# Optimization experiments

Hardware: AMD Instinct MI355X
Metric: run time of the kernel (lower is better)

Reference implementation:

```python
import jax, jax.numpy as jnp
import numpy as np
import math

D_MODEL = 1024
N_HEADS = 16
HEAD_DIM = D_MODEL // N_HEADS
B, S = 4, 4096


def setup_inputs() -> dict:
    key = jax.random.key(0)
    ks = jax.random.split(key, 8)
    # xavier-uniform-ish scale for square DxD matrices
    lim = math.sqrt(6.0 / (D_MODEL + D_MODEL))
    def W(k):
        return jax.random.uniform(k, (D_MODEL, D_MODEL), jnp.float32, -lim, lim)
    return {
        "x": jax.random.normal(ks[0], (B, S, D_MODEL), jnp.float32),
        "fractal_dim": jnp.float32(1.7),
        "Wq": W(ks[1]), "bq": jnp.zeros((D_MODEL,), jnp.float32),
        "Wk": W(ks[2]), "bk": jnp.zeros((D_MODEL,), jnp.float32),
        "Wv": W(ks[3]), "bv": jnp.zeros((D_MODEL,), jnp.float32),
        "Wo": W(ks[4]), "bo": jnp.zeros((D_MODEL,), jnp.float32),
        "alpha": jnp.float32(1.5),
        "frac_scale": jnp.float32(0.5),
    }


def reference(x, fractal_dim, Wq, bq, Wk, bk, Wv, bv, Wo, bo, alpha, frac_scale):
    b, s, d = x.shape
    h, hd = N_HEADS, HEAD_DIM
    residual = x

    adaptive_alpha = alpha + frac_scale * (fractal_dim - 1.5)

    q = (x @ Wq + bq).reshape(b, s, h, hd)
    k = (x @ Wk + bk).reshape(b, s, h, hd)
    v = (x @ Wv + bv).reshape(b, s, h, hd)

    # spectral filter over frequency axis (seq dim)
    freqs = jnp.fft.fftfreq(s).astype(x.dtype)  # [S]
    phase = adaptive_alpha * jnp.arctan(jnp.log(jnp.abs(freqs) + 1e-10))
    filt = jnp.exp(1j * phase)[None, :, None, None]  # [1,S,1,1] complex

    def spectral(t):
        tf = jnp.fft.fft(t, axis=1, norm="ortho") * filt
        return jnp.fft.ifft(tf, axis=1, norm="ortho").real

    q_t, k_t, v_t = spectral(q), spectral(k), spectral(v)

    # per-(token) dot product across head_dim -> logits over heads
    logits = jnp.einsum("bshd,bshd->bsh", q_t, k_t) / math.sqrt(hd)
    w = jax.nn.softmax(logits, axis=-1)  # softmax over heads
    attended = w[..., None] * v_t  # [B,S,H,Hd]

    # final inverse FFT of the (real) attended signal along seq dim
    attended_time = jnp.fft.ifft(attended.astype(jnp.complex64), axis=1, norm="ortho").real

    out = attended_time.reshape(b, s, d) @ Wo + bo
    return out + residual
```

## Files before the change

### kernel.cpp

```cpp
#include <hip/hip_runtime.h>

#define S      4096
#define DM     1024
#define NB     4
#define NH     16
#define HDIM   64
#define MTOT   (NB * S)
#define DS     ((long)DM * S)
#define MH     2304
#define KH     2112
#define KH2    2112
#define MEO    2048

typedef __attribute__((ext_vector_type(8))) short short8;
typedef __attribute__((ext_vector_type(4))) float f32x4;
typedef __attribute__((ext_vector_type(8))) unsigned short u16x8;
typedef __attribute__((ext_vector_type(4))) unsigned short u16x4;

__device__ __forceinline__ unsigned short f2bf(float f) {
  union { float f; unsigned u; } v; v.f = f;
  unsigned r = v.u + 0x7fffu + ((v.u >> 16) & 1u);
  return (unsigned short)(r >> 16);
}
__device__ __forceinline__ float bf2f(short h) {
  union { unsigned u; float f; } v; v.u = ((unsigned)(unsigned short)h) << 16;
  return v.f;
}

#define GLOAD(gp, lp) __builtin_amdgcn_global_load_lds( \
    (const __attribute__((address_space(1))) void*)(gp), \
    (__attribute__((address_space(3))) void*)(lp), 16, 0, 0)

#define SBAR() do { asm volatile("" ::: "memory"); __builtin_amdgcn_s_barrier(); \
                    asm volatile("" ::: "memory"); } while (0)
#define WAITL0() asm volatile("s_waitcnt lgkmcnt(0)" ::: "memory")

#define SWZ(o) ((o) ^ ((((o) >> 7) & 3) << 4))


__global__ void k_tables(const float* __restrict__ fd, const float* __restrict__ alpha,
                         const float* __restrict__ fsc,
                         float* __restrict__ cos_tab, float* __restrict__ c_arr) {
  int k = blockIdx.x * 256 + threadIdx.x;
  if (k >= S) return;
  float aa = alpha[0] + fsc[0] * (fd[0] - 1.5f);
  const float twopi = 6.28318530717958647692f;
  cos_tab[k] = cosf(twopi * ((float)k / (float)S));
  int kk = (k <= S / 2) ? k : (S - k);
  float af = (float)kk / (float)S;
  c_arr[k] = cosf(aa * atanf(logf(af + 1e-10f)));
}

__global__ void k_g(const float* __restrict__ cos_tab, const float* __restrict__ c_arr,
                    float* __restrict__ g) {
  __shared__ float sct[S];
  __shared__ float sc[S];
  __shared__ float red[16][17];
  for (int i = threadIdx.x; i < S; i += 256) { sct[i] = cos_tab[i]; sc[i] = c_arr[i]; }
  __syncthreads();
  int jl = threadIdx.x >> 4, r = threadIdx.x & 15;
  int j = blockIdx.x * 16 + jl;
  float acc = 0.f;
#pragma unroll 4
  for (int i = 0; i < 256; ++i) {
    int k = r + 16 * i;
    acc += sc[k] * sct[(j * k) & (S - 1)];
  }
  red[jl][r] = acc;
  __syncthreads();
  if (r == 0) {
    float s = 0.f;
#pragma unroll
    for (int i = 0; i < 16; ++i) s += red[jl][i];
    g[j] = s * (1.f / (float)S);
  }
}

__global__ void k_buildEO(const float* __restrict__ g, short* __restrict__ Ge) {
  long i8 = ((long)blockIdx.x * 256 + threadIdx.x) * 8;
  if (i8 >= (long)MEO * KH2) return;
  int n = (int)(i8 / KH2);
  int m = (int)(i8 % KH2);
  u16x8 ev, ov;
#pragma unroll
  for (int j = 0; j < 8; ++j) {
    int mm = m + j;
    float e, o;
    if (mm == 0)            { e = g[n]; o = 0.f; }
    else if (mm == 2048)    { e = g[(n + 2048) & (S - 1)]; o = 0.f; }
    else if (mm > 2048)     { e = 0.f; o = 0.f; }
    else {
      float a = g[(n - mm) & (S - 1)], b = g[(n + mm) & (S - 1)];
      e = 0.5f * (a + b); o = 0.5f * (a - b);
    }
    ev[j] = f2bf(e); ov[j] = f2bf(o);
  }
  *(u16x8*)(Ge + i8) = ev;
  *(u16x8*)(Ge + (long)MEO * KH2 + i8) = ov;
}

__global__ void k_foldT(const float* __restrict__ x, short* __restrict__ uv) {
  __shared__ float tp[64][65];
  __shared__ float tm[64][65];
  int m0 = blockIdx.x * 64, d0 = blockIdx.y * 64, b = blockIdx.z;
  int t = threadIdx.x;
  int r = t >> 4, c4 = (t & 15) * 4;
#pragma unroll
  for (int rr = 0; rr < 4; ++rr) {
    int m = m0 + r + rr * 16;
    float4 vp = *(const float4*)(x + ((long)(b * S + m)) * DM + d0 + c4);
    int ms = (S - m) & (S - 1);
    float4 vm = *(const float4*)(x + ((long)(b * S + ms)) * DM + d0 + c4);
    tp[r + rr * 16][c4 + 0] = vp.x; tp[r + rr * 16][c4 + 1] = vp.y;
    tp[r + rr * 16][c4 + 2] = vp.z; tp[r + rr * 16][c4 + 3] = vp.w;
    tm[r + rr * 16][c4 + 0] = vm.x; tm[r + rr * 16][c4 + 1] = vm.y;
    tm[r + rr * 16][c4 + 2] = vm.z; tm[r + rr * 16][c4 + 3] = vm.w;
  }
  __syncthreads();
  int m_loc = t & 63, dq = t >> 6;
#pragma unroll
  for (int i = 0; i < 16; ++i) {
    int d_loc = dq * 16 + i;
    int m = m0 + m_loc;
    float P = tp[m_loc][d_loc], M = tm[m_loc][d_loc];
    float u, v;
    if (m == 0 || m == 2048) { u = P; v = 0.f; }
    else if (m > 2048)       { u = 0.f; v = 0.f; }
    else                     { u = P + M; v = P - M; }
    long base = ((long)(b * DM + d0 + d_loc)) * KH2 + m;
    uv[base] = (short)f2bf(u);
    uv[base + (long)4 * DM * KH2] = (short)f2bf(v);
  }
}

__global__ void k_row2048(const float* __restrict__ g, const short* __restrict__ uv,
                          short* __restrict__ Xs) {
  __shared__ float red[256];
  int bd = blockIdx.x;
  int b = bd >> 10, d = bd & (DM - 1);
  const short* up = uv + ((long)(b * DM + d)) * KH2;
  int t = threadIdx.x;
  float acc = 0.f;
  for (int m = t; m <= 2048; m += 256)
    acc += g[2048 - m] * bf2f(up[m]);
  red[t] = acc;
  __syncthreads();
  for (int sh = 128; sh > 0; sh >>= 1) {
    if (t < sh) red[t] += red[t + sh];
    __syncthreads();
  }
  if (t == 0) Xs[((long)b * S + 2048) * DM + d] = (short)f2bf(red[0]);
}

__global__ void k_unfold(const short* __restrict__ AB, short* __restrict__ Xs) {
  long i8 = ((long)blockIdx.x * 256 + threadIdx.x) * 8;
  if (i8 >= (long)NB * MEO * DM) return;
  int b = (int)(i8 >> 21);
  long rr = i8 & ((1L << 21) - 1);
  int n = (int)(rr >> 10);
  int d = (int)(rr & (DM - 1));
  u16x8 av = *(const u16x8*)(AB + i8);
  u16x8 bv = *(const u16x8*)(AB + ((long)4 * MEO * DM) + i8);
  u16x8 sv, dv;
#pragma unroll
  for (int j = 0; j < 8; ++j) {
    float A = bf2f((short)av[j]), B = bf2f((short)bv[j]);
    sv[j] = f2bf(A + B);
    dv[j] = f2bf(A - B);
  }
  *(u16x8*)(Xs + ((long)b * S + n) * DM + d) = sv;
  if (n > 0)
    *(u16x8*)(Xs + ((long)b * S + (S - n)) * DM + d) = dv;
}

__global__ void k_buildM2(const float* __restrict__ cos_tab, short* __restrict__ Mc2) {
  long i8 = ((long)blockIdx.x * 256 + threadIdx.x) * 8;
  if (i8 >= (long)MH * KH) return;
  int n = (int)(i8 / KH);
  int m = (int)(i8 % KH);
  u16x8 mv;
#pragma unroll
  for (int j = 0; j < 8; ++j) {
    int mm = m + j;
    float vv = (mm <= 2048) ? cos_tab[(n * mm) & (S - 1)] * 0.015625f : 0.f;
    mv[j] = f2bf(vv);
  }
  *(u16x8*)(Mc2 + i8) = mv;
}

__global__ void k_transW(const float* __restrict__ W, short* __restrict__ WT) {
  __shared__ float tile[64][65];
  int k0 = blockIdx.x * 64, n0 = blockIdx.y * 64;
  int t = threadIdx.x;
  int r = t >> 4, c4 = (t & 15) * 4;
  const float* ip = W + (long)k0 * DM + n0;
#pragma unroll
  for (int rr = 0; rr < 4; ++rr) {
    float4 v = *(const float4*)(ip + (long)(r + rr * 16) * DM + c4);
    tile[r + rr * 16][c4 + 0] = v.x;
    tile[r + rr * 16][c4 + 1] = v.y;
    tile[r + rr * 16][c4 + 2] = v.z;
    tile[r + rr * 16][c4 + 3] = v.w;
  }
  __syncthreads();
  int k_loc = t & 63, nq = t >> 6;
  short* op = WT + (long)n0 * DM + k0;
#pragma unroll
  for (int i = 0; i < 16; ++i) {
    int n_loc = nq * 16 + i;
    op[(long)n_loc * DM + k_loc] = (short)f2bf(tile[k_loc][n_loc]);
  }
}

__global__ void k_logits(const short* __restrict__ Qt, const short* __restrict__ Kt,
                         float* __restrict__ logits) {
  int s = blockIdx.x * 256 + threadIdx.x;
  int h = blockIdx.y, b = blockIdx.z;
  const short* q = Qt + ((long)b * DM + h * HDIM) * S + s;
  const short* k = Kt + ((long)b * DM + h * HDIM) * S + s;
  float acc = 0.f;
#pragma unroll 8
  for (int j = 0; j < HDIM; ++j)
    acc += bf2f(q[(long)j * S]) * bf2f(k[(long)j * S]);
  logits[((long)b * NH + h) * S + s] = acc * 0.125f;
}

__global__ void k_softw(const float* __restrict__ logits, float* __restrict__ w) {
  int idx = blockIdx.x * 256 + threadIdx.x;
  if (idx >= NB * S) return;
  int b = idx >> 12, s = idx & (S - 1);
  const float* lp = logits + (long)b * NH * S + s;
  float v[NH];
  float m = -1e30f;
#pragma unroll
  for (int h = 0; h < NH; ++h) { v[h] = lp[(long)h * S]; m = fmaxf(m, v[h]); }
  float sum = 0.f;
#pragma unroll
  for (int h = 0; h < NH; ++h) { v[h] = expf(v[h] - m); sum += v[h]; }
  float inv = 1.f / sum;
  float* wp = w + (long)b * NH * S + s;
#pragma unroll
  for (int h = 0; h < NH; ++h) wp[(long)h * S] = v[h] * inv;
}

__global__ void k_attfold(const short* __restrict__ vt, const float* __restrict__ wsm,
                          short* __restrict__ A2t) {
  int m = blockIdx.x * 256 + threadIdx.x;
  if (m >= KH) return;
  int d = blockIdx.y, b = blockIdx.z;
  const short* vp = vt + ((long)b * DM + d) * S;
  const float* wp = wsm + ((long)b * NH + (d >> 6)) * S;
  float v;
  if (m == 0) v = wp[0] * bf2f(vp[0]);
  else if (m < 2048) v = wp[m] * bf2f(vp[m]) + wp[4096 - m] * bf2f(vp[4096 - m]);
  else if (m == 2048) v = wp[2048] * bf2f(vp[2048]);
  else v = 0.f;
  A2t[((long)b * DM + d) * KH + m] = (short)f2bf(v);
}

template <int EPI, int AMIR = 0, int ASEL = 0, int WALK = 0>
__global__ __launch_bounds__(512, 2) void gemm8(
    const short* __restrict__ A, const short* __restrict__ Bt,
    short* __restrict__ Cb, short* __restrict__ Cb2, short* __restrict__ Cb3,
    float* __restrict__ Cf,
    const float* __restrict__ bias, const float* __restrict__ bias2,
    const float* __restrict__ bias3,
    const float* __restrict__ bsc, const float* __restrict__ resid,
    int M, int N, int K, long aBatch, long bBatch, long cBatch) {
  __shared__ __align__(16) short SH[65536];
  auto Ab = [&](int buf, int ks) { return SH + (buf * 2 + ks) * 8192; };
  auto Bb = [&](int buf, int ks) { return SH + 32768 + (buf * 2 + ks) * 8192; };

  const int gx = gridDim.x, gy = gridDim.y;
  const int nwg = gx * gy * gridDim.z;
  int lin = blockIdx.x + gx * (blockIdx.y + gy * blockIdx.z);
  int wg = lin;
  if ((nwg & 7) == 0) {
    const int cpx = nwg >> 3;
    wg = (lin & 7) * cpx + (lin >> 3);
  }
  const int NTN = N >> 8;
  const int NTM = M >> 8;
  int ntile, mtile, bz;
  if (WALK) {
    mtile = wg % NTM;
    const int rest = wg / NTM;
    ntile = rest % NTN;
    bz = rest / NTN;
  } else {
    ntile = wg % NTN;
    const int rest = wg / NTN;
    mtile = rest % NTM;
    bz = rest / NTM;
  }

  const short* Ag = ASEL ? (A + (long)(bz >> 2) * aBatch) : (A + (long)bz * aBatch);
  const short* Bg = Bt + (long)bz * bBatch;
  const int m0 = mtile << 8, n0 = ntile << 8;
  const int tid = threadIdx.x;
  const int lane = tid & 63;
  const int wid = tid >> 6;
  const int wm = wid >> 2, wn = wid & 3;

  f32x4 acc[8][4];
#pragma unroll
  for (int i = 0; i < 8; ++i)
#pragma unroll
    for (int j = 0; j < 4; ++j) acc[i][j] = (f32x4){0.f, 0.f, 0.f, 0.f};

  const int NT = K >> 6;
  auto stage = [&](int h) {
    const int tau = h >> 2, q = h & 3;
    const int buf = tau & 1, ks = q >> 1;
    short* ldsbase = (q & 1) ? Bb(buf, ks) : Ab(buf, ks);
    const short* gsrc = (q & 1) ? Bg : Ag;
    const int row0 = (q & 1) ? n0 : m0;
    const long k0 = (long)tau * 64 + ks * 32;
#pragma unroll
    for (int j = 0; j < 2; ++j) {
      const int o = tid * 16 + j * 8192;
      const int lo = SWZ(o);
      const int row = lo >> 6;
      const int cs = (lo & 63) >> 1;
      const short* gp;
      if (AMIR && !(q & 1)) {
        int grow = row0 + row;
        int b_ = grow >> 12, s_ = grow & (S - 1);
        int sm = (s_ <= 2048) ? s_ : (4096 - s_);
        gp = Ag + ((long)b_ * MH + sm) * K + k0 + cs;
      } else {
        gp = gsrc + (long)(row0 + row) * K + k0 + cs;
      }
      GLOAD(gp, (short*)((char*)ldsbase + o));
    }
  };

  for (int h = 0; h < 7; ++h) stage(h);
  asm volatile("s_waitcnt vmcnt(6)" ::: "memory");
  SBAR();

  short8 bf[4];
  for (int t = 0; t < NT; ++t) {
    const int buf = t & 1;
#pragma unroll
    for (int p = 0; p < 4; ++p) {
      const int ks = p >> 1, mh = p & 1;
      short8 af[4];
      {
        const short* Ah = Ab(buf, ks);
        const int kb = (lane >> 4) * 16;
        const int r0 = wm * 128 + mh * 64 + (lane & 15);
#pragma unroll
        for (int i = 0; i < 4; ++i) {
          int byte = (r0 + i * 16) * 64 + kb;
          byte = SWZ(byte);
          af[i] = *(const short8*)((const char*)Ah + byte);
        }
        if (mh == 0) {
          const short* Bh = Bb(buf, ks);
          const int c0 = wn * 64 + (lane & 15);
#pragma unroll
          for (int j = 0; j < 4; ++j) {
            int byte = (c0 + j * 16) * 64 + kb;
            byte = SWZ(byte);
            bf[j] = *(const short8*)((const char*)Bh + byte);
          }
        }
      }
      { const int h = 4 * t + p + 7; if (h < 4 * NT) stage(h); }
      SBAR();
      WAITL0();
      __builtin_amdgcn_s_setprio(1);
#pragma unroll
      for (int i = 0; i < 4; ++i)
#pragma unroll
        for (int j = 0; j < 4; ++j)
          acc[mh * 4 + i][j] = __builtin_amdgcn_mfma_f32_16x16x32_bf16(
              af[i], bf[j], acc[mh * 4 + i][j], 0, 0, 0);
      __builtin_amdgcn_s_setprio(0);
      if (p == 3) {
        if (t < NT - 2) {
          asm volatile("s_waitcnt vmcnt(6)" ::: "memory");
        } else if (t == NT - 2) {
          asm volatile("s_waitcnt vmcnt(0)" ::: "memory");
        }
      }
      SBAR();
    }
  }

  const int rl = (lane >> 4) << 2;

  if constexpr (EPI == 3) {
    const int b_ = m0 >> 12;
    const int s0 = m0 & (S - 1);
    const int pidx = n0 >> 10;
    const int d0 = n0 & (DM - 1);
    const float* bp = (pidx == 0) ? bias : ((pidx == 1) ? bias2 : bias3);
    short* Cp = (pidx == 0) ? Cb : ((pidx == 1) ? Cb2 : Cb3);
    const float sc = bsc ? bsc[0] : 1.f;
#pragma unroll
    for (int f = 0; f < 8; ++f) {
      const int lr0 = wm * 128 + f * 16 + rl;
#pragma unroll
      for (int j = 0; j < 4; ++j) {
        const int lc = wn * 64 + j * 16 + (lane & 15);
        const float bi = bp[d0 + lc] * sc;
        f32x4 a = acc[f][j];
        u16x4 pk;
#pragma unroll
        for (int r = 0; r < 4; ++r) pk[r] = f2bf(a[r] + bi);
        int ad = lc * 512 + lr0 * 2;
        ad ^= (lc & 7) << 4;
        *(u16x4*)((char*)SH + ad) = pk;
      }
    }
    __syncthreads();
    const long gbase = ((long)(b_ * DM + d0)) * S + s0;
#pragma unroll
    for (int it = 0; it < 16; ++it) {
      const int lc = wid * 32 + (it << 1) + (lane >> 5);
      const int lr = (lane & 31) * 8;
      int ad = lc * 512 + lr * 2;
      ad ^= (lc & 7) << 4;
      u16x8 vv = *(u16x8*)((char*)SH + ad);
      *(u16x8*)(Cp + gbase + (long)lc * S + lr) = vv;
    }
    return;
  }

#pragma unroll
  for (int f = 0; f < 8; ++f) {
    const int rbase = m0 + wm * 128 + f * 16 + rl;
#pragma unroll
    for (int j = 0; j < 4; ++j) {
      const int col = n0 + wn * 64 + j * 16 + (lane & 15);
      f32x4 a = acc[f][j];
      if constexpr (EPI == 0) {
        short* cp = Cb + (long)bz * cBatch;
#pragma unroll
        for (int r = 0; r < 4; ++r)
          cp[(long)(rbase + r) * N + col] = (short)f2bf(a[r]);
      } else {
        float bi = bias[col];
#pragma unroll
        for (int r = 0; r < 4; ++r) {
          long o = (long)(rbase + r) * N + col;
          Cf[o] = a[r] + bi + resid[o];
        }
      }
    }
  }
}

extern "C" void kernel_launch(void* const* d_in, const int* in_sizes, int n_in,
                              void* d_out, int out_size, void* d_ws, size_t ws_size,
                              hipStream_t stream) {
  const float* x     = (const float*)d_in[0];
  const float* fd    = (const float*)d_in[1];
  const float* Wq    = (const float*)d_in[2];
  const float* bq    = (const float*)d_in[3];
  const float* Wk    = (const float*)d_in[4];
  const float* bk    = (const float*)d_in[5];
  const float* Wv    = (const float*)d_in[6];
  const float* bv    = (const float*)d_in[7];
  const float* Wo    = (const float*)d_in[8];
  const float* bo    = (const float*)d_in[9];
  const float* alpha = (const float*)d_in[10];
  const float* fsc   = (const float*)d_in[11];
  float* out = (float*)d_out;

  char* wp = (char*)d_ws;
  auto alloc = [&](size_t bytes) {
    char* p = wp;
    wp += (bytes + 255) & ~(size_t)255;
    return p;
  };
  float* cos_tab = (float*)alloc(S * 4);
  float* c_arr   = (float*)alloc(S * 4);
  float* g       = (float*)alloc(S * 4);
  float* logits  = (float*)alloc((size_t)NB * NH * S * 4);
  float* wsm     = (float*)alloc((size_t)NB * NH * S * 4);
  short* WTcat = (short*)alloc((size_t)3 * DM * DM * 2);
  short* WoT   = (short*)alloc((size_t)DM * DM * 2);
  short* slotA = (short*)alloc((size_t)NB * DS * 2);
  short* slotB = (short*)alloc((size_t)NB * DS * 2);
  short* slotC = (short*)alloc((size_t)NB * DS * 2);

  short* uv  = (short*)d_out;
  short* QtT = (short*)d_out;
  short* KtT = (short*)d_out + (size_t)2 * DS;

  short* Ge  = slotB;
  short* ABout = slotA;
  short* Xs  = slotC;
  short* VtT = slotA;
  short* Mc2 = slotB;
  short* A2t = (short*)((char*)slotB + 10u * 1024 * 1024);
  short* att_half = slotC;

  dim3 blk(256), blk8(512);

  k_tables<<<dim3(S / 256), blk, 0, stream>>>(fd, alpha, fsc, cos_tab, c_arr);
  k_g<<<dim3(S / 16), blk, 0, stream>>>(cos_tab, c_arr, g);
  k_buildEO<<<dim3((unsigned)((long)MEO * KH2 / 8 / 256)), blk, 0, stream>>>(g, Ge);
  k_foldT<<<dim3(33, DM / 64, NB), blk, 0, stream>>>(x, uv);

  k_transW<<<dim3(16, 16), blk, 0, stream>>>(Wq, WTcat);
  k_transW<<<dim3(16, 16), blk, 0, stream>>>(Wk, WTcat + (size_t)DM * DM);
  k_transW<<<dim3(16, 16), blk, 0, stream>>>(Wv, WTcat + (size_t)2 * DM * DM);
  k_transW<<<dim3(16, 16), blk, 0, stream>>>(Wo, WoT);

  dim3 geo(DM / 256, MEO / 256, 8);
  gemm8<0, 0, 1><<<geo, blk8, 0, stream>>>(Ge, uv, ABout, nullptr, nullptr, nullptr,
                                           nullptr, nullptr, nullptr, nullptr, nullptr,
                                           MEO, DM, KH2,
                                           (long)MEO * KH2, (long)DM * KH2, (long)MEO * DM);
  k_row2048<<<dim3(NB * DM), blk, 0, stream>>>(g, uv, Xs);
  k_unfold<<<dim3((unsigned)((long)NB * MEO * DM / 8 / 256)), blk, 0, stream>>>(ABout, Xs);

  dim3 gqkv(3 * DM / 256, MTOT / 256, 1);
  gemm8<3><<<gqkv, blk8, 0, stream>>>(Xs, WTcat, QtT, KtT, VtT, nullptr,
                                      bq, bk, bv, c_arr, nullptr,
                                      MTOT, 3 * DM, DM, 0, 0, 0);

  k_logits<<<dim3(S / 256, NH, NB), blk, 0, stream>>>(QtT, KtT, logits);
  k_softw<<<dim3(NB * S / 256), blk, 0, stream>>>(logits, wsm);
  k_attfold<<<dim3(KH / 256 + 1, DM, NB), blk, 0, stream>>>(VtT, wsm, A2t);

  k_buildM2<<<dim3((unsigned)((long)MH * KH / 8 / 256)), blk, 0, stream>>>(cos_tab, Mc2);
  dim3 ghalf(DM / 256, MH / 256, NB);
  gemm8<0><<<ghalf, blk8, 0, stream>>>(Mc2, A2t, att_half, nullptr, nullptr, nullptr,
                                       nullptr, nullptr, nullptr, nullptr, nullptr,
                                       MH, DM, KH, 0, (long)DM * KH, (long)MH * DM);

  dim3 gproj(DM / 256, MTOT / 256, 1);
  gemm8<2, 1><<<gproj, blk8, 0, stream>>>(att_half, WoT, nullptr, nullptr, nullptr, out,
                                          bo, nullptr, nullptr, nullptr, x,
                                          MTOT, DM, DM, 0, 0, 0);
}
```

Baseline: 413.8 us.

## Fuse logits+softmax, merge small kernels, switch QKV output to token-major layout

Result: no change. 410.7 us (-0.7%).

```diff
diff --git a/kernel.cpp b/kernel.cpp
--- a/kernel.cpp
+++ b/kernel.cpp
@@ -133,44 +133,44 @@
   }
 }
 
-__global__ void k_row2048(const float* __restrict__ g, const short* __restrict__ uv,
-                          short* __restrict__ Xs) {
+__global__ void k_unfold2(const short* __restrict__ AB, const float* __restrict__ g,
+                          const short* __restrict__ uv, short* __restrict__ Xs) {
   __shared__ float red[256];
-  int bd = blockIdx.x;
-  int b = bd >> 10, d = bd & (DM - 1);
-  const short* up = uv + ((long)(b * DM + d)) * KH2;
-  int t = threadIdx.x;
-  float acc = 0.f;
-  for (int m = t; m <= 2048; m += 256)
-    acc += g[2048 - m] * bf2f(up[m]);
-  red[t] = acc;
-  __syncthreads();
-  for (int sh = 128; sh > 0; sh >>= 1) {
-    if (t < sh) red[t] += red[t + sh];
+  int bx = blockIdx.x;
+  if (bx < 4096) {
+    long i8 = ((long)bx * 256 + threadIdx.x) * 8;
+    int b = (int)(i8 >> 21);
+    long rr = i8 & ((1L << 21) - 1);
+    int n = (int)(rr >> 10);
+    int d = (int)(rr & (DM - 1));
+    u16x8 av = *(const u16x8*)(AB + i8);
+    u16x8 bv = *(const u16x8*)(AB + ((long)4 * MEO * DM) + i8);
+    u16x8 sv, dv;
+#pragma unroll
+    for (int j = 0; j < 8; ++j) {
+      float A = bf2f((short)av[j]), B = bf2f((short)bv[j]);
+      sv[j] = f2bf(A + B);
+      dv[j] = f2bf(A - B);
+    }
+    *(u16x8*)(Xs + ((long)b * S + n) * DM + d) = sv;
+    if (n > 0)
+      *(u16x8*)(Xs + ((long)b * S + (S - n)) * DM + d) = dv;
+  } else {
+    int bd = bx - 4096;
+    int b = bd >> 10, d = bd & (DM - 1);
+    const short* up = uv + ((long)(b * DM + d)) * KH2;
+    int t = threadIdx.x;
+    float acc = 0.f;
+    for (int m = t; m <= 2048; m += 256)
+      acc += g[2048 - m] * bf2f(up[m]);
+    red[t] = acc;
     __syncthreads();
-  }
-  if (t == 0) Xs[((long)b * S + 2048) * DM + d] = (short)f2bf(red[0]);
-}
-
-__global__ void k_unfold(const short* __restrict__ AB, short* __restrict__ Xs) {
-  long i8 = ((long)blockIdx.x * 256 + threadIdx.x) * 8;
-  if (i8 >= (long)NB * MEO * DM) return;
-  int b = (int)(i8 >> 21);
-  long rr = i8 & ((1L << 21) - 1);
-  int n = (int)(rr >> 10);
-  int d = (int)(rr & (DM - 1));
-  u16x8 av = *(const u16x8*)(AB + i8);
-  u16x8 bv = *(const u16x8*)(AB + ((long)4 * MEO * DM) + i8);
-  u16x8 sv, dv;
-#pragma unroll
-  for (int j = 0; j < 8; ++j) {
-    float A = bf2f((short)av[j]), B = bf2f((short)bv[j]);
-    sv[j] = f2bf(A + B);
-    dv[j] = f2bf(A - B);
-  }
-  *(u16x8*)(Xs + ((long)b * S + n) * DM + d) = sv;
-  if (n > 0)
-    *(u16x8*)(Xs + ((long)b * S + (S - n)) * DM + d) = dv;
+    for (int sh = 128; sh > 0; sh >>= 1) {
+      if (t < sh) red[t] += red[t + sh];
+      __syncthreads();
+    }
+    if (t == 0) Xs[((long)b * S + 2048) * DM + d] = (short)f2bf(red[0]);
+  }
 }
 
 __global__ void k_buildM2(const float* __restrict__ cos_tab, short* __restrict__ Mc2) {
@@ -188,8 +188,13 @@
   *(u16x8*)(Mc2 + i8) = mv;
 }
 
-__global__ void k_transW(const float* __restrict__ W, short* __restrict__ WT) {
+__global__ void k_transW4(const float* __restrict__ W0, const float* __restrict__ W1,
+                          const float* __restrict__ W2, const float* __restrict__ W3,
+                          short* __restrict__ WT) {
   __shared__ float tile[64][65];
+  int z = blockIdx.z;
+  const float* W = (z == 0) ? W0 : ((z == 1) ? W1 : ((z == 2) ? W2 : W3));
+  short* WTo = WT + (size_t)z * DM * DM;
   int k0 = blockIdx.x * 64, n0 = blockIdx.y * 64;
   int t = threadIdx.x;
   int r = t >> 4, c4 = (t & 15) * 4;
@@ -204,7 +209,7 @@
   }
   __syncthreads();
   int k_loc = t & 63, nq = t >> 6;
-  short* op = WT + (long)n0 * DM + k0;
+  short* op = WTo + (long)n0 * DM + k0;
 #pragma unroll
   for (int i = 0; i < 16; ++i) {
     int n_loc = nq * 16 + i;
@@ -212,50 +217,71 @@
   }
 }
 
-__global__ void k_logits(const short* __restrict__ Qt, const short* __restrict__ Kt,
-                         float* __restrict__ logits) {
-  int s = blockIdx.x * 256 + threadIdx.x;
-  int h = blockIdx.y, b = blockIdx.z;
-  const short* q = Qt + ((long)b * DM + h * HDIM) * S + s;
-  const short* k = Kt + ((long)b * DM + h * HDIM) * S + s;
+__global__ void k_logsoft(const short* __restrict__ Q, const short* __restrict__ K,
+                          float* __restrict__ w) {
+  int idx = blockIdx.x * 16 + (threadIdx.x >> 4);
+  int h = threadIdx.x & 15;
+  const short* q = Q + (long)idx * DM + h * HDIM;
+  const short* k = K + (long)idx * DM + h * HDIM;
   float acc = 0.f;
-#pragma unroll 8
-  for (int j = 0; j < HDIM; ++j)
-    acc += bf2f(q[(long)j * S]) * bf2f(k[(long)j * S]);
-  logits[((long)b * NH + h) * S + s] = acc * 0.125f;
-}
-
-__global__ void k_softw(const float* __restrict__ logits, float* __restrict__ w) {
-  int idx = blockIdx.x * 256 + threadIdx.x;
-  if (idx >= NB * S) return;
+#pragma unroll
+  for (int jj = 0; jj < 8; ++jj) {
+    u16x8 qa = *(const u16x8*)(q + jj * 8);
+    u16x8 ka = *(const u16x8*)(k + jj * 8);
+#pragma unroll
+    for (int l = 0; l < 8; ++l) acc += bf2f((short)qa[l]) * bf2f((short)ka[l]);
+  }
+  acc *= 0.125f;
+  float m = acc;
+#pragma unroll
+  for (int d = 1; d < 16; d <<= 1) m = fmaxf(m, __shfl_xor(m, d, 16));
+  float e = expf(acc - m);
+  float ssum = e;
+#pragma unroll
+  for (int d = 1; d < 16; d <<= 1) ssum += __shfl_xor(ssum, d, 16);
   int b = idx >> 12, s = idx & (S - 1);
-  const float* lp = logits + (long)b * NH * S + s;
-  float v[NH];
-  float m = -1e30f;
-#pragma unroll
-  for (int h = 0; h < NH; ++h) { v[h] = lp[(long)h * S]; m = fmaxf(m, v[h]); }
-  float sum = 0.f;
-#pragma unroll
-  for (int h = 0; h < NH; ++h) { v[h] = expf(v[h] - m); sum += v[h]; }
-  float inv = 1.f / sum;
-  float* wp = w + (long)b * NH * S + s;
-#pragma unroll
-  for (int h = 0; h < NH; ++h) wp[(long)h * S] = v[h] * inv;
-}
-
-__global__ void k_attfold(const short* __restrict__ vt, const float* __restrict__ wsm,
-                          short* __restrict__ A2t) {
-  int m = blockIdx.x * 256 + threadIdx.x;
-  if (m >= KH) return;
-  int d = blockIdx.y, b = blockIdx.z;
-  const short* vp = vt + ((long)b * DM + d) * S;
-  const float* wp = wsm + ((long)b * NH + (d >> 6)) * S;
-  float v;
-  if (m == 0) v = wp[0] * bf2f(vp[0]);
-  else if (m < 2048) v = wp[m] * bf2f(vp[m]) + wp[4096 - m] * bf2f(vp[4096 - m]);
-  else if (m == 2048) v = wp[2048] * bf2f(vp[2048]);
-  else v = 0.f;
-  A2t[((long)b * DM + d) * KH + m] = (short)f2bf(v);
+  w[((long)b * NH + h) * S + s] = e / ssum;
+}
+
+__global__ void k_attfold2(const short* __restrict__ V, const float* __restrict__ wsm,
+                           short* __restrict__ A2t) {
+  __shared__ float t1[64][65];
+  __shared__ float t2[64][65];
+  __shared__ float w1[64], w2[64];
+  int m0 = blockIdx.x * 64, d0 = blockIdx.y * 64, b = blockIdx.z;
+  int t = threadIdx.x;
+  int h0 = d0 >> 6;
+  if (t < 64) {
+    int m = m0 + t;
+    const float* wp = wsm + ((long)b * NH + h0) * S;
+    w1[t] = wp[m & (S - 1)];
+    w2[t] = wp[(S - m) & (S - 1)];
+  }
+  int r = t >> 4, c4 = (t & 15) * 4;
+#pragma unroll
+  for (int rr = 0; rr < 4; ++rr) {
+    int i = r + rr * 16;
+    int m = m0 + i;
+    u16x4 a = *(const u16x4*)(V + ((long)(b * S + (m & (S - 1)))) * DM + d0 + c4);
+    u16x4 bb = *(const u16x4*)(V + ((long)(b * S + ((S - m) & (S - 1)))) * DM + d0 + c4);
+#pragma unroll
+    for (int l = 0; l < 4; ++l) {
+      t1[i][c4 + l] = bf2f((short)a[l]);
+      t2[i][c4 + l] = bf2f((short)bb[l]);
+    }
+  }
+  __syncthreads();
+  int i_loc = t & 63, jq = t >> 6;
+  int m = m0 + i_loc;
+#pragma unroll
+  for (int jj = 0; jj < 16; ++jj) {
+    int j = jq * 16 + jj;
+    float rv;
+    if (m == 0 || m == 2048) rv = w1[i_loc] * t1[i_loc][j];
+    else if (m < 2048)       rv = w1[i_loc] * t1[i_loc][j] + w2[i_loc] * t2[i_loc][j];
+    else                     rv = 0.f;
+    A2t[((long)(b * DM + d0 + j)) * KH + m] = (short)f2bf(rv);
+  }
 }
 
 template <int EPI, int AMIR = 0, int ASEL = 0, int WALK = 0>
@@ -390,45 +416,6 @@
   }
 
   const int rl = (lane >> 4) << 2;
-
-  if constexpr (EPI == 3) {
-    const int b_ = m0 >> 12;
-    const int s0 = m0 & (S - 1);
-    const int pidx = n0 >> 10;
-    const int d0 = n0 & (DM - 1);
-    const float* bp = (pidx == 0) ? bias : ((pidx == 1) ? bias2 : bias3);
-    short* Cp = (pidx == 0) ? Cb : ((pidx == 1) ? Cb2 : Cb3);
-    const float sc = bsc ? bsc[0] : 1.f;
-#pragma unroll
-    for (int f = 0; f < 8; ++f) {
-      const int lr0 = wm * 128 + f * 16 + rl;
-#pragma unroll
-      for (int j = 0; j < 4; ++j) {
-        const int lc = wn * 64 + j * 16 + (lane & 15);
-        const float bi = bp[d0 + lc] * sc;
-        f32x4 a = acc[f][j];
-        u16x4 pk;
-#pragma unroll
-        for (int r = 0; r < 4; ++r) pk[r] = f2bf(a[r] + bi);
-        int ad = lc * 512 + lr0 * 2;
-        ad ^= (lc & 7) << 4;
-        *(u16x4*)((char*)SH + ad) = pk;
-      }
-    }
-    __syncthreads();
-    const long gbase = ((long)(b_ * DM + d0)) * S + s0;
-#pragma unroll
-    for (int it = 0; it < 16; ++it) {
-      const int lc = wid * 32 + (it << 1) + (lane >> 5);
-      const int lr = (lane & 31) * 8;
-      int ad = lc * 512 + lr * 2;
-      ad ^= (lc & 7) << 4;
-      u16x8 vv = *(u16x8*)((char*)SH + ad);
-      *(u16x8*)(Cp + gbase + (long)lc * S + lr) = vv;
-    }
-    return;
-  }
-
 #pragma unroll
   for (int f = 0; f < 8; ++f) {
     const int rbase = m0 + wm * 128 + f * 16 + rl;
@@ -441,6 +428,15 @@
 #pragma unroll
         for (int r = 0; r < 4; ++r)
           cp[(long)(rbase + r) * N + col] = (short)f2bf(a[r]);
+      } else if constexpr (EPI == 4) {
+        const int pidx = col >> 10;
+        const int dcol = col & (DM - 1);
+        short* Cp = (pidx == 0) ? Cb : ((pidx == 1) ? Cb2 : Cb3);
+        const float* bp = (pidx == 0) ? bias : ((pidx == 1) ? bias2 : bias3);
+        const float bi = bp[dcol] * (bsc ? bsc[0] : 1.f);
+#pragma unroll
+        for (int r = 0; r < 4; ++r)
+          Cp[(long)(rbase + r) * DM + dcol] = (short)f2bf(a[r] + bi);
       } else {
         float bi = bias[col];
 #pragma unroll
@@ -479,22 +475,21 @@
   float* cos_tab = (float*)alloc(S * 4);
   float* c_arr   = (float*)alloc(S * 4);
   float* g       = (float*)alloc(S * 4);
-  float* logits  = (float*)alloc((size_t)NB * NH * S * 4);
   float* wsm     = (float*)alloc((size_t)NB * NH * S * 4);
-  short* WTcat = (short*)alloc((size_t)3 * DM * DM * 2);
-  short* WoT   = (short*)alloc((size_t)DM * DM * 2);
+  short* WTcat = (short*)alloc((size_t)4 * DM * DM * 2);
+  short* WoT   = WTcat + (size_t)3 * DM * DM;
   short* slotA = (short*)alloc((size_t)NB * DS * 2);
   short* slotB = (short*)alloc((size_t)NB * DS * 2);
   short* slotC = (short*)alloc((size_t)NB * DS * 2);
 
-  short* uv  = (short*)d_out;
-  short* QtT = (short*)d_out;
-  short* KtT = (short*)d_out + (size_t)2 * DS;
+  short* uv = (short*)d_out;
+  short* Qn = (short*)d_out;
+  short* Kn = (short*)d_out + (size_t)NB * DS;
 
   short* Ge  = slotB;
   short* ABout = slotA;
   short* Xs  = slotC;
-  short* VtT = slotA;
+  short* Vn  = slotA;
   short* Mc2 = slotB;
   short* A2t = (short*)((char*)slotB + 10u * 1024 * 1024);
   short* att_half = slotC;
@@ -505,28 +500,22 @@
   k_g<<<dim3(S / 16), blk, 0, stream>>>(cos_tab, c_arr, g);
   k_buildEO<<<dim3((unsigned)((long)MEO * KH2 / 8 / 256)), blk, 0, stream>>>(g, Ge);
   k_foldT<<<dim3(33, DM / 64, NB), blk, 0, stream>>>(x, uv);
-
-  k_transW<<<dim3(16, 16), blk, 0, stream>>>(Wq, WTcat);
-  k_transW<<<dim3(16, 16), blk, 0, stream>>>(Wk, WTcat + (size_t)DM * DM);
-  k_transW<<<dim3(16, 16), blk, 0, stream>>>(Wv, WTcat + (size_t)2 * DM * DM);
-  k_transW<<<dim3(16, 16), blk, 0, stream>>>(Wo, WoT);
+  k_transW4<<<dim3(16, 16, 4), blk, 0, stream>>>(Wq, Wk, Wv, Wo, WTcat);
 
   dim3 geo(DM / 256, MEO / 256, 8);
   gemm8<0, 0, 1><<<geo, blk8, 0, stream>>>(Ge, uv, ABout, nullptr, nullptr, nullptr,
                                            nullptr, nullptr, nullptr, nullptr, nullptr,
                                            MEO, DM, KH2,
                                            (long)MEO * KH2, (long)DM * KH2, (long)MEO * DM);
-  k_row2048<<<dim3(NB * DM), blk, 0, stream>>>(g, uv, Xs);
-  k_unfold<<<dim3((unsigned)((long)NB * MEO * DM / 8 / 256)), blk, 0, stream>>>(ABout, Xs);
+  k_unfold2<<<dim3(8192), blk, 0, stream>>>(ABout, g, uv, Xs);
 
   dim3 gqkv(3 * DM / 256, MTOT / 256, 1);
-  gemm8<3><<<gqkv, blk8, 0, stream>>>(Xs, WTcat, QtT, KtT, VtT, nullptr,
+  gemm8<4><<<gqkv, blk8, 0, stream>>>(Xs, WTcat, Qn, Kn, Vn, nullptr,
                                       bq, bk, bv, c_arr, nullptr,
                                       MTOT, 3 * DM, DM, 0, 0, 0);
 
-  k_logits<<<dim3(S / 256, NH, NB), blk, 0, stream>>>(QtT, KtT, logits);
-  k_softw<<<dim3(NB * S / 256), blk, 0, stream>>>(logits, wsm);
-  k_attfold<<<dim3(KH / 256 + 1, DM, NB), blk, 0, stream>>>(VtT, wsm, A2t);
+  k_logsoft<<<dim3(MTOT / 16), blk, 0, stream>>>(Qn, Kn, wsm);
+  k_attfold2<<<dim3(KH / 64, DM / 64, NB), blk, 0, stream>>>(Vn, wsm, A2t);
 
   k_buildM2<<<dim3((unsigned)((long)MH * KH / 8 / 256)), blk, 0, stream>>>(cos_tab, Mc2);
   dim3 ghalf(DM / 256, MH / 256, NB);
```
